# Kernel optimization log

Measured on AMD Instinct MI355X. Metric: run time of the kernel, lower is better.

The kernel has to match this reference:

```python
import jax, jax.numpy as jnp
import numpy as np
jax.config.update("jax_enable_x64", True)

T, C, F = 2048, 2048, 8192
f32 = jnp.float32
f64 = jnp.float64


def setup_inputs() -> dict:
    key = jax.random.key(0)
    ks = jax.random.split(key, 20)
    s = 0.02
    return {
        "x": jax.random.normal(ks[0], (T, C), f32),
        "att_shift": jnp.zeros((C,), f32),
        "wkv_state": jnp.zeros((2, C), f32),
        "ffn_shift": jnp.zeros((C,), f32),
        "ln1_w": jnp.ones((C,), f32),
        "ln1_b": jnp.zeros((C,), f32),
        "ln2_w": jnp.ones((C,), f32),
        "ln2_b": jnp.zeros((C,), f32),
        "time_mix_k": jax.random.uniform(ks[1], (C,), f32),
        "time_mix_v": jax.random.uniform(ks[2], (C,), f32),
        "time_mix_r": jax.random.uniform(ks[3], (C,), f32),
        "time_decay": jax.random.normal(ks[4], (C,), f32) * 0.5,
        "time_first": jax.random.normal(ks[5], (C,), f32) * 0.5,
        "att_key": jax.random.normal(ks[6], (C, C), f32) * s,
        "att_value": jax.random.normal(ks[7], (C, C), f32) * s,
        "att_receptance": jax.random.normal(ks[8], (C, C), f32) * s,
        "att_output": jax.random.normal(ks[9], (C, C), f32) * s,
        "ffn_time_mix_k": jax.random.uniform(ks[10], (C,), f32),
        "ffn_time_mix_r": jax.random.uniform(ks[11], (C,), f32),
        "ffn_key": jax.random.normal(ks[12], (F, C), f32) * s,
        "ffn_value": jax.random.normal(ks[13], (C, F), f32) * s,
        "ffn_receptance": jax.random.normal(ks[14], (C, C), f32) * s,
    }


def _ln(x, w, b):
    m = x.mean(-1, keepdims=True)
    v = x.var(-1, keepdims=True)
    return (x - m) * jax.lax.rsqrt(v + 1e-5) * w + b


def _wkv(time_decay, time_first, k, v, wkv_state):
    # faithful to wkv_mop: double-precision math, float32 state round-trip per step
    u = time_first.astype(f64)
    w = -jnp.exp(time_decay.astype(f64))
    ew = jnp.exp(w)

    def step(carry, kv_t):
        a, b = carry  # float32 states [C]
        k_t, v_t = kv_t
        kd = k_t.astype(f64)
        vd = v_t.astype(f64)
        e = jnp.exp(u + w + kd)
        y = (a + e * vd) / (b + e)
        kk = jnp.exp(kd)
        a2 = ((a + kk * vd) * ew).astype(f32)
        b2 = ((b + kk) * ew).astype(f32)
        return (a2, b2), y.astype(f32)

    _, y = jax.lax.scan(step, (wkv_state[0], wkv_state[1]), (k, v))
    return y  # [T, C]


def reference(x, att_shift, wkv_state, ffn_shift, ln1_w, ln1_b, ln2_w, ln2_b,
              time_mix_k, time_mix_v, time_mix_r, time_decay, time_first,
              att_key, att_value, att_receptance, att_output,
              ffn_time_mix_k, ffn_time_mix_r, ffn_key, ffn_value, ffn_receptance):
    # --- TimeMix (att) on rx = ln1(x); shiftamount=2 -> prev token of rx ---
    rx = _ln(x, ln1_w, ln1_b)                         # [T, C]
    xx = jnp.concatenate([att_shift[None, :], rx[:-1]], axis=0)
    xk = rx * time_mix_k + xx * (1.0 - time_mix_k)
    xv = rx * time_mix_v + xx * (1.0 - time_mix_v)
    xr = rx * time_mix_r + xx * (1.0 - time_mix_r)
    k = xk @ att_key.T                                # [T, C]
    v = xv @ att_value.T
    sr = jax.nn.sigmoid(xr @ att_receptance.T)
    y = _wkv(time_decay, time_first, k, v, wkv_state)
    x = x + (sr * y) @ att_output.T
    # --- ChannelMix (ffn) on fx = ln2(x); shift = prev token of fx ---
    fx = _ln(x, ln2_w, ln2_b)
    fxx = jnp.concatenate([ffn_shift[None, :], fx[:-1]], axis=0)
    fk = fx * ffn_time_mix_k + fxx * (1.0 - ffn_time_mix_k)
    fr = fx * ffn_time_mix_r + fxx * (1.0 - ffn_time_mix_r)
    kf = jnp.square(jax.nn.relu(fk @ ffn_key.T))      # [T, F]
    kv = kf @ ffn_value.T                             # [T, C]
    out = x + jax.nn.sigmoid(fr @ ffn_receptance.T) * kv
    return out
```

## Files before the change

kernel.cpp:

```cpp
#include <hip/hip_runtime.h>
#include <hip/hip_bf16.h>

typedef unsigned short u16;
typedef short bf16x8 __attribute__((ext_vector_type(8)));
typedef float f32x4 __attribute__((ext_vector_type(4)));

#define T_DIM 2048
#define C_DIM 2048
#define F_DIM 8192
#define WKV_L 32
#define WKV_P (T_DIM / WKV_L)

__device__ __forceinline__ u16 f2bf(float f) {
    unsigned int u = __float_as_uint(f);
    u += 0x7fff + ((u >> 16) & 1);
    return (u16)(u >> 16);
}

__device__ __forceinline__ void async16(const void* g, void* l) {
    __builtin_amdgcn_global_load_lds(
        (__attribute__((address_space(1))) const unsigned int*)g,
        (__attribute__((address_space(3))) unsigned int*)l, 16, 0, 0);
}

__global__ __launch_bounds__(256) void ln_mix3(
        const float* __restrict__ x, const float* __restrict__ sh,
        const float* __restrict__ w, const float* __restrict__ b,
        const float* __restrict__ mk, const float* __restrict__ mv,
        const float* __restrict__ mr,
        u16* __restrict__ xk, u16* __restrict__ xv, u16* __restrict__ xr) {
    __shared__ float red[16];
    const int t = blockIdx.x, tid = threadIdx.x;
    const float4* cr = (const float4*)(x + (size_t)t * C_DIM);
    float4 c0 = cr[tid * 2], c1 = cr[tid * 2 + 1];
    float s = c0.x + c0.y + c0.z + c0.w + c1.x + c1.y + c1.z + c1.w;
    float q = c0.x * c0.x + c0.y * c0.y + c0.z * c0.z + c0.w * c0.w
            + c1.x * c1.x + c1.y * c1.y + c1.z * c1.z + c1.w * c1.w;
    float4 p0, p1;
    float sp = 0.f, qp = 0.f;
    if (t > 0) {
        const float4* pr = (const float4*)(x + (size_t)(t - 1) * C_DIM);
        p0 = pr[tid * 2]; p1 = pr[tid * 2 + 1];
        sp = p0.x + p0.y + p0.z + p0.w + p1.x + p1.y + p1.z + p1.w;
        qp = p0.x * p0.x + p0.y * p0.y + p0.z * p0.z + p0.w * p0.w
           + p1.x * p1.x + p1.y * p1.y + p1.z * p1.z + p1.w * p1.w;
    } else {
        const float4* pr = (const float4*)sh;
        p0 = pr[tid * 2]; p1 = pr[tid * 2 + 1];
    }
    #pragma unroll
    for (int off = 32; off > 0; off >>= 1) {
        s += __shfl_down(s, off);   q += __shfl_down(q, off);
        sp += __shfl_down(sp, off); qp += __shfl_down(qp, off);
    }
    const int lane = tid & 63, wv = tid >> 6;
    if (lane == 0) { red[wv] = s; red[4 + wv] = q; red[8 + wv] = sp; red[12 + wv] = qp; }
    __syncthreads();
    if (tid == 0) {
        red[0] += red[1] + red[2] + red[3];
        red[4] += red[5] + red[6] + red[7];
        red[8] += red[9] + red[10] + red[11];
        red[12] += red[13] + red[14] + red[15];
    }
    __syncthreads();
    const float mc = red[0] * (1.f / C_DIM);
    const float ic = rsqrtf(red[4] * (1.f / C_DIM) - mc * mc + 1e-5f);
    const float mp = red[8] * (1.f / C_DIM);
    const float ip = rsqrtf(red[12] * (1.f / C_DIM) - mp * mp + 1e-5f);
    const float4* w4 = (const float4*)w;
    const float4* b4 = (const float4*)b;
    #pragma unroll
    for (int j = 0; j < 2; ++j) {
        const int i4 = tid * 2 + j;
        float4 cv = j ? c1 : c0, pv = j ? p1 : p0;
        float4 wv4 = w4[i4], bv = b4[i4];
        float4 cl, pl;
        cl.x = (cv.x - mc) * ic * wv4.x + bv.x;
        cl.y = (cv.y - mc) * ic * wv4.y + bv.y;
        cl.z = (cv.z - mc) * ic * wv4.z + bv.z;
        cl.w = (cv.w - mc) * ic * wv4.w + bv.w;
        if (t > 0) {
            pl.x = (pv.x - mp) * ip * wv4.x + bv.x;
            pl.y = (pv.y - mp) * ip * wv4.y + bv.y;
            pl.z = (pv.z - mp) * ip * wv4.z + bv.z;
            pl.w = (pv.w - mp) * ip * wv4.w + bv.w;
        } else pl = pv;
        const size_t o = (size_t)t * (C_DIM / 4) + i4;
        float4 m;
        ushort4 r;
        m = ((const float4*)mk)[i4];
        r.x = f2bf(cl.x * m.x + pl.x * (1.f - m.x));
        r.y = f2bf(cl.y * m.y + pl.y * (1.f - m.y));
        r.z = f2bf(cl.z * m.z + pl.z * (1.f - m.z));
        r.w = f2bf(cl.w * m.w + pl.w * (1.f - m.w));
        ((ushort4*)xk)[o] = r;
        m = ((const float4*)mv)[i4];
        r.x = f2bf(cl.x * m.x + pl.x * (1.f - m.x));
        r.y = f2bf(cl.y * m.y + pl.y * (1.f - m.y));
        r.z = f2bf(cl.z * m.z + pl.z * (1.f - m.z));
        r.w = f2bf(cl.w * m.w + pl.w * (1.f - m.w));
        ((ushort4*)xv)[o] = r;
        m = ((const float4*)mr)[i4];
        r.x = f2bf(cl.x * m.x + pl.x * (1.f - m.x));
        r.y = f2bf(cl.y * m.y + pl.y * (1.f - m.y));
        r.z = f2bf(cl.z * m.z + pl.z * (1.f - m.z));
        r.w = f2bf(cl.w * m.w + pl.w * (1.f - m.w));
        ((ushort4*)xr)[o] = r;
    }
}

__global__ __launch_bounds__(256) void ln_mix2(
        const float* __restrict__ x, const float* __restrict__ sh,
        const float* __restrict__ w, const float* __restrict__ b,
        const float* __restrict__ mk, const float* __restrict__ mr,
        u16* __restrict__ fk, u16* __restrict__ fr) {
    __shared__ float red[16];
    const int t = blockIdx.x, tid = threadIdx.x;
    const float4* cr = (const float4*)(x + (size_t)t * C_DIM);
    float4 c0 = cr[tid * 2], c1 = cr[tid * 2 + 1];
    float s = c0.x + c0.y + c0.z + c0.w + c1.x + c1.y + c1.z + c1.w;
    float q = c0.x * c0.x + c0.y * c0.y + c0.z * c0.z + c0.w * c0.w
            + c1.x * c1.x + c1.y * c1.y + c1.z * c1.z + c1.w * c1.w;
    float4 p0, p1;
    float sp = 0.f, qp = 0.f;
    if (t > 0) {
        const float4* pr = (const float4*)(x + (size_t)(t - 1) * C_DIM);
        p0 = pr[tid * 2]; p1 = pr[tid * 2 + 1];
        sp = p0.x + p0.y + p0.z + p0.w + p1.x + p1.y + p1.z + p1.w;
        qp = p0.x * p0.x + p0.y * p0.y + p0.z * p0.z + p0.w * p0.w
           + p1.x * p1.x + p1.y * p1.y + p1.z * p1.z + p1.w * p1.w;
    } else {
        const float4* pr = (const float4*)sh;
        p0 = pr[tid * 2]; p1 = pr[tid * 2 + 1];
    }
    #pragma unroll
    for (int off = 32; off > 0; off >>= 1) {
        s += __shfl_down(s, off);   q += __shfl_down(q, off);
        sp += __shfl_down(sp, off); qp += __shfl_down(qp, off);
    }
    const int lane = tid & 63, wv = tid >> 6;
    if (lane == 0) { red[wv] = s; red[4 + wv] = q; red[8 + wv] = sp; red[12 + wv] = qp; }
    __syncthreads();
    if (tid == 0) {
        red[0] += red[1] + red[2] + red[3];
        red[4] += red[5] + red[6] + red[7];
        red[8] += red[9] + red[10] + red[11];
        red[12] += red[13] + red[14] + red[15];
    }
    __syncthreads();
    const float mc = red[0] * (1.f / C_DIM);
    const float ic = rsqrtf(red[4] * (1.f / C_DIM) - mc * mc + 1e-5f);
    const float mp = red[8] * (1.f / C_DIM);
    const float ip = rsqrtf(red[12] * (1.f / C_DIM) - mp * mp + 1e-5f);
    const float4* w4 = (const float4*)w;
    const float4* b4 = (const float4*)b;
    #pragma unroll
    for (int j = 0; j < 2; ++j) {
        const int i4 = tid * 2 + j;
        float4 cv = j ? c1 : c0, pv = j ? p1 : p0;
        float4 wv4 = w4[i4], bv = b4[i4];
        float4 cl, pl;
        cl.x = (cv.x - mc) * ic * wv4.x + bv.x;
        cl.y = (cv.y - mc) * ic * wv4.y + bv.y;
        cl.z = (cv.z - mc) * ic * wv4.z + bv.z;
        cl.w = (cv.w - mc) * ic * wv4.w + bv.w;
        if (t > 0) {
            pl.x = (pv.x - mp) * ip * wv4.x + bv.x;
            pl.y = (pv.y - mp) * ip * wv4.y + bv.y;
            pl.z = (pv.z - mp) * ip * wv4.z + bv.z;
            pl.w = (pv.w - mp) * ip * wv4.w + bv.w;
        } else pl = pv;
        const size_t o = (size_t)t * (C_DIM / 4) + i4;
        float4 m;
        ushort4 r;
        m = ((const float4*)mk)[i4];
        r.x = f2bf(cl.x * m.x + pl.x * (1.f - m.x));
        r.y = f2bf(cl.y * m.y + pl.y * (1.f - m.y));
        r.z = f2bf(cl.z * m.z + pl.z * (1.f - m.z));
        r.w = f2bf(cl.w * m.w + pl.w * (1.f - m.w));
        ((ushort4*)fk)[o] = r;
        m = ((const float4*)mr)[i4];
        r.x = f2bf(cl.x * m.x + pl.x * (1.f - m.x));
        r.y = f2bf(cl.y * m.y + pl.y * (1.f - m.y));
        r.z = f2bf(cl.z * m.z + pl.z * (1.f - m.z));
        r.w = f2bf(cl.w * m.w + pl.w * (1.f - m.w));
        ((ushort4*)fr)[o] = r;
    }
}

__global__ __launch_bounds__(256) void cvt_bf16(const float* __restrict__ in,
                                                u16* __restrict__ out, int n8) {
    int i = blockIdx.x * 256 + threadIdx.x;
    const int stride = gridDim.x * 256;
    for (; i < n8; i += stride) {
        const float4* p = (const float4*)(in + (size_t)i * 8);
        float4 a = p[0], b = p[1];
        ushort4 lo, hi;
        lo.x = f2bf(a.x); lo.y = f2bf(a.y); lo.z = f2bf(a.z); lo.w = f2bf(a.w);
        hi.x = f2bf(b.x); hi.y = f2bf(b.y); hi.z = f2bf(b.z); hi.w = f2bf(b.w);
        ((ushort4*)out)[i * 2] = lo;
        ((ushort4*)out)[i * 2 + 1] = hi;
    }
}

__global__ __launch_bounds__(256) void cvt4_bf16(const float* __restrict__ i0,
                                                 const float* __restrict__ i1,
                                                 const float* __restrict__ i2,
                                                 const float* __restrict__ i3,
                                                 u16* __restrict__ out, int n8) {
    const int sel = blockIdx.y;
    const float* in = sel == 0 ? i0 : (sel == 1 ? i1 : (sel == 2 ? i2 : i3));
    u16* o = out + (size_t)sel * n8 * 8;
    int i = blockIdx.x * 256 + threadIdx.x;
    const int stride = gridDim.x * 256;
    for (; i < n8; i += stride) {
        const float4* p = (const float4*)(in + (size_t)i * 8);
        float4 a = p[0], b = p[1];
        ushort4 lo, hi;
        lo.x = f2bf(a.x); lo.y = f2bf(a.y); lo.z = f2bf(a.z); lo.w = f2bf(a.w);
        hi.x = f2bf(b.x); hi.y = f2bf(b.y); hi.z = f2bf(b.z); hi.w = f2bf(b.w);
        ((ushort4*)o)[i * 2] = lo;
        ((ushort4*)o)[i * 2 + 1] = hi;
    }
}

__global__ __launch_bounds__(256) void reduce2(const float* __restrict__ p0,
                                               const float* __restrict__ p1,
                                               float* __restrict__ o, int n4) {
    int i = blockIdx.x * 256 + threadIdx.x;
    const int stride = gridDim.x * 256;
    for (; i < n4; i += stride) {
        float4 a = ((const float4*)p0)[i], b = ((const float4*)p1)[i];
        float4 r;
        r.x = a.x + b.x;
        r.y = a.y + b.y;
        r.z = a.z + b.z;
        r.w = a.w + b.w;
        ((float4*)o)[i] = r;
    }
}

__global__ __launch_bounds__(256) void wkv_part(const float* __restrict__ td,
                                                const float* __restrict__ k,
                                                const float* __restrict__ v,
                                                float* __restrict__ Ab,
                                                float* __restrict__ Bb) {
    const int idx = blockIdx.x * 256 + threadIdx.x;
    const int c = idx & (C_DIM - 1);
    const int p = idx >> 11;
    const float ew = expf(-expf(td[c]));
    float A = 0.f, B = 0.f;
    size_t o = (size_t)(p * WKV_L) * C_DIM + c;
    #pragma unroll 4
    for (int i = 0; i < WKV_L; ++i, o += C_DIM) {
        const float kk = expf(k[o]);
        A = (A + kk * v[o]) * ew;
        B = (B + kk) * ew;
    }
    Ab[p * C_DIM + c] = A;
    Bb[p * C_DIM + c] = B;
}

__global__ __launch_bounds__(256) void wkv_comb(const float* __restrict__ td,
                                                const float* __restrict__ st,
                                                const float* __restrict__ Ab,
                                                const float* __restrict__ Bb,
                                                float* __restrict__ Sa,
                                                float* __restrict__ Sb) {
    const int c = blockIdx.x * 256 + threadIdx.x;
    const float w = -expf(td[c]);
    const float dL = expf(w * (float)WKV_L);
    float a = st[c];
    float b = st[C_DIM + c];
    #pragma unroll 4
    for (int p = 0; p < WKV_P; ++p) {
        Sa[p * C_DIM + c] = a;
        Sb[p * C_DIM + c] = b;
        a = dL * a + Ab[p * C_DIM + c];
        b = dL * b + Bb[p * C_DIM + c];
    }
}

__global__ __launch_bounds__(256) void wkv_emit(const float* __restrict__ td,
                                                const float* __restrict__ tf,
                                                const float* __restrict__ k,
                                                const float* __restrict__ v,
                                                const float* __restrict__ r,
                                                const float* __restrict__ Sa,
                                                const float* __restrict__ Sb,
                                                u16* __restrict__ pout) {
    const int idx = blockIdx.x * 256 + threadIdx.x;
    const int c = idx & (C_DIM - 1);
    const int p = idx >> 11;
    const float u = tf[c];
    const float w = -expf(td[c]);
    const float ew = expf(w);
    float a = Sa[p * C_DIM + c];
    float b = Sb[p * C_DIM + c];
    size_t o = (size_t)(p * WKV_L) * C_DIM + c;
    #pragma unroll 2
    for (int i = 0; i < WKV_L; ++i, o += C_DIM) {
        const float kt = k[o], vt = v[o], rt = r[o];
        const float e = expf(u + w + kt);
        const float y = (a + e * vt) / (b + e);
        const float kk = expf(kt);
        a = (a + kk * vt) * ew;
        b = (b + kk) * ew;
        const float sr = 1.f / (1.f + expf(-rt));
        pout[o] = f2bf(sr * y);
    }
}

enum { EPI_F32 = 0, EPI_ADDX = 1, EPI_RELU2 = 2, EPI_SIGMULADD = 3 };

template <int EPI>
__global__ __launch_bounds__(256, 3) void gemm_bt(
        const u16* __restrict__ A, int lda, long a_zs,
        const u16* __restrict__ B, int ldb, long b_zs,
        long koff, int Kloop,
        void* __restrict__ outp, int ldo, long o_zs,
        const float* __restrict__ aux1, const float* __restrict__ aux2) {
    __shared__ u16 lds[3 * 8192];
    const int tid = threadIdx.x;
    const int l = tid & 63, w = tid >> 6;
    const int wr2 = w >> 1, wc2 = w & 1;

    const int gx = gridDim.x, gy = gridDim.y;
    const int nxy = gx * gy;
    const int flat = (blockIdx.z * gy + blockIdx.y) * gx + blockIdx.x;
    const int cpx = (nxy * gridDim.z) >> 3;
    const int swz = (flat & 7) * cpx + (flat >> 3);
    const int z = swz / nxy;
    const int rem = swz - z * nxy;
    const int bm = rem % gy;
    const int bn = rem / gy;

    const u16* Ag = A + (size_t)z * a_zs + (size_t)z * koff + (size_t)bm * 128 * lda;
    const u16* Bg = B + (size_t)z * b_zs + (size_t)z * koff + (size_t)bn * 128 * ldb;

    long gA[2], gB[2];
    int dA[2], dB[2];
    #pragma unroll
    for (int j = 0; j < 2; ++j) {
        const int off = j * 4096 + w * 1024 + l * 16;
        const int row = off >> 6;
        const int cb = (off & 63) ^ (((off >> 9) & 1) << 5);
        gA[j] = (long)row * lda + (cb >> 1);
        gB[j] = (long)row * ldb + (cb >> 1);
        dA[j] = j * 2048 + w * 512;
        dB[j] = 4096 + j * 2048 + w * 512;
    }

    int offA[4], offB[4];
    #pragma unroll
    for (int m = 0; m < 4; ++m) {
        const int lin = (wr2 * 64 + m * 16 + (l & 15)) * 64 + ((l >> 4) << 4);
        offA[m] = (lin ^ (((lin >> 9) & 1) << 5)) >> 1;
    }
    #pragma unroll
    for (int n = 0; n < 4; ++n) {
        const int lin = (wc2 * 64 + n * 16 + (l & 15)) * 64 + ((l >> 4) << 4);
        offB[n] = 4096 + ((lin ^ (((lin >> 9) & 1) << 5)) >> 1);
    }

    const f32x4 fz = {0.f, 0.f, 0.f, 0.f};
    f32x4 acc[4][4];
    #pragma unroll
    for (int m = 0; m < 4; ++m)
        #pragma unroll
        for (int n = 0; n < 4; ++n) acc[m][n] = fz;

    const int NT = Kloop >> 5;

    auto stage = [&](int kt, int sp) {
        const long ko = (long)kt << 5;
        const int sb = sp * 8192;
        async16(Ag + gA[0] + ko, &lds[sb + dA[0]]);
        async16(Ag + gA[1] + ko, &lds[sb + dA[1]]);
        async16(Bg + gB[0] + ko, &lds[sb + dB[0]]);
        async16(Bg + gB[1] + ko, &lds[sb + dB[1]]);
    };

    stage(0, 0);
    stage(1, 1);

    int sr = 0;
    for (int t = 0; t < NT; ++t) {
        asm volatile("s_waitcnt vmcnt(4)" ::: "memory");
        __builtin_amdgcn_s_barrier();
        __builtin_amdgcn_sched_barrier(0);
        {
            const int tp = (t + 2 < NT) ? t + 2 : NT - 1;
            const int sp = (sr == 0) ? 2 : sr - 1;
            stage(tp, sp);
        }
        const int sb = sr * 8192;
        bf16x8 af[4], bfv[4];
        #pragma unroll
        for (int m = 0; m < 4; ++m) af[m] = *(const bf16x8*)&lds[sb + offA[m]];
        #pragma unroll
        for (int n = 0; n < 4; ++n) bfv[n] = *(const bf16x8*)&lds[sb + offB[n]];
        __builtin_amdgcn_s_setprio(1);
        #pragma unroll
        for (int m = 0; m < 2; ++m)
            #pragma unroll
            for (int n = 0; n < 4; ++n)
                acc[m][n] = __builtin_amdgcn_mfma_f32_16x16x32_bf16(af[m], bfv[n], acc[m][n], 0, 0, 0);
        __builtin_amdgcn_s_setprio(0);
        __builtin_amdgcn_s_setprio(1);
        #pragma unroll
        for (int m = 2; m < 4; ++m)
            #pragma unroll
            for (int n = 0; n < 4; ++n)
                acc[m][n] = __builtin_amdgcn_mfma_f32_16x16x32_bf16(af[m], bfv[n], acc[m][n], 0, 0, 0);
        __builtin_amdgcn_s_setprio(0);
        sr = (sr == 2) ? 0 : sr + 1;
    }
    asm volatile("s_waitcnt vmcnt(0)" ::: "memory");

    const int r00 = bm * 128 + wr2 * 64 + ((l >> 4) << 2);
    const int c00 = bn * 128 + wc2 * 64 + (l & 15);
    #pragma unroll
    for (int m = 0; m < 4; ++m) {
        #pragma unroll
        for (int n = 0; n < 4; ++n) {
            #pragma unroll
            for (int j = 0; j < 4; ++j) {
                const int rr = r00 + m * 16 + j;
                const int cc = c00 + n * 16;
                const size_t o = (size_t)rr * ldo + cc;
                const float val = acc[m][n][j];
                if constexpr (EPI == EPI_F32) {
                    ((float*)outp)[(size_t)z * o_zs + o] = val;
                } else if constexpr (EPI == EPI_ADDX) {
                    ((float*)outp)[o] = aux1[o] + val;
                } else if constexpr (EPI == EPI_RELU2) {
                    const float tp2 = fmaxf(val, 0.f);
                    ((u16*)outp)[o] = f2bf(tp2 * tp2);
                } else {
                    const float sg = 1.f / (1.f + expf(-val));
                    ((float*)outp)[o] = aux1[o] + sg * aux2[o];
                }
            }
        }
    }
}

extern "C" void kernel_launch(void* const* d_in, const int* in_sizes, int n_in,
                              void* d_out, int out_size, void* d_ws, size_t ws_size,
                              hipStream_t stream) {
    const float* x         = (const float*)d_in[0];
    const float* att_shift = (const float*)d_in[1];
    const float* wkv_state = (const float*)d_in[2];
    const float* ffn_shift = (const float*)d_in[3];
    const float* ln1w = (const float*)d_in[4];
    const float* ln1b = (const float*)d_in[5];
    const float* ln2w = (const float*)d_in[6];
    const float* ln2b = (const float*)d_in[7];
    const float* tmk  = (const float*)d_in[8];
    const float* tmv  = (const float*)d_in[9];
    const float* tmr  = (const float*)d_in[10];
    const float* td   = (const float*)d_in[11];
    const float* tf   = (const float*)d_in[12];
    const float* Wk   = (const float*)d_in[13];
    const float* Wv   = (const float*)d_in[14];
    const float* Wr   = (const float*)d_in[15];
    const float* Wo   = (const float*)d_in[16];
    const float* ftmk = (const float*)d_in[17];
    const float* ftmr = (const float*)d_in[18];
    const float* Wfk  = (const float*)d_in[19];
    const float* Wfv  = (const float*)d_in[20];
    const float* Wfr  = (const float*)d_in[21];
    float* out = (float*)d_out;

    char* ws = (char*)d_ws;
    const size_t MB = 1ull << 20;
    float* rx0 = (float*)(ws + 0);
    u16*   xk  = (u16*)(ws + 16 * MB);
    u16*   xv  = (u16*)(ws + 24 * MB);
    u16*   xr  = (u16*)(ws + 32 * MB);
    float* kb  = (float*)(ws + 40 * MB);
    float* vb  = (float*)(ws + 56 * MB);
    float* rb  = (float*)(ws + 72 * MB);
    u16*   pb  = (u16*)(ws + 88 * MB);
    float* x1  = (float*)(ws + 96 * MB);
    u16*   kf  = (u16*)(ws + 112 * MB);
    u16*   Wb  = (u16*)(ws + 144 * MB);
    float* wAb = (float*)(ws + 112 * MB);
    float* wBb = (float*)(ws + 112 * MB + 512 * 1024);
    float* wSa = (float*)(ws + 113 * MB);
    float* wSb = (float*)(ws + 113 * MB + 512 * 1024);
    float* fvp = (float*)(ws + 32 * MB);

    const int T = T_DIM, C = C_DIM, F = F_DIM;
    const dim3 blk(256);

    ln_mix3<<<T, blk, 0, stream>>>(x, att_shift, ln1w, ln1b, tmk, tmv, tmr, xk, xv, xr);

    cvt4_bf16<<<dim3(1024, 4), blk, 0, stream>>>(Wk, Wv, Wr, Wo, Wb, C * C / 8);
    gemm_bt<EPI_F32><<<dim3(C / 128, T / 128, 3), blk, 0, stream>>>(
        xk, C, (long)T * C, Wb, C, (long)C * C, 0, C,
        kb, C, (long)T * C, nullptr, nullptr);

    wkv_part<<<(C * WKV_P) / 256, blk, 0, stream>>>(td, kb, vb, wAb, wBb);
    wkv_comb<<<C / 256, blk, 0, stream>>>(td, wkv_state, wAb, wBb, wSa, wSb);
    wkv_emit<<<(C * WKV_P) / 256, blk, 0, stream>>>(td, tf, kb, vb, rb, wSa, wSb, pb);

    gemm_bt<EPI_ADDX><<<dim3(C / 128, T / 128, 1), blk, 0, stream>>>(
        pb, C, 0, Wb + 3 * (size_t)C * C, C, 0, 0, C, x1, C, 0, x, nullptr);

    ln_mix2<<<T, blk, 0, stream>>>(x1, ffn_shift, ln2w, ln2b, ftmk, ftmr, xk, xv);

    cvt_bf16<<<2048, blk, 0, stream>>>(Wfk, Wb, F * C / 8);
    gemm_bt<EPI_RELU2><<<dim3(F / 128, T / 128, 1), blk, 0, stream>>>(
        xk, C, 0, Wb, C, 0, 0, C, kf, F, 0, nullptr, nullptr);

    cvt_bf16<<<2048, blk, 0, stream>>>(Wfv, Wb, C * F / 8);
    gemm_bt<EPI_F32><<<dim3(C / 128, T / 128, 2), blk, 0, stream>>>(
        kf, F, 0, Wb, F, 0, 4096, 4096, fvp, C, (long)T * C, nullptr, nullptr);
    reduce2<<<2048, blk, 0, stream>>>(fvp, fvp + (size_t)T * C, rx0, T * C / 4);

    cvt_bf16<<<2048, blk, 0, stream>>>(Wfr, Wb, C * C / 8);
    gemm_bt<EPI_SIGMULADD><<<dim3(C / 128, T / 128, 1), blk, 0, stream>>>(
        xv, C, 0, Wb, C, 0, 0, C, out, C, 0, x1, rx0);
}
```

Baseline: 412.3 us.

## Add 256x256 8-wave pipelined GEMM for FFN matmuls with 4-way split-K

Adds a new bf16 MFMA GEMM kernel for the two large FFN matmuls. It uses 256x256 output tiles, 512 threads and double-buffered LDS fed by async global-to-LDS loads. It interleaves LDS fragment reads, staging of the next K tile and MFMA quads under barriers and raised wave priority, and swizzles the block order across groups of 8. The ffn_value GEMM moves from 2-way to 4-way split-K to keep enough blocks with the larger tiles, and a reduce4 kernel sums the four partials. The cost is extra partial-buffer traffic, a larger workspace footprint and heavy register use from 32 accumulators per lane.

```diff
diff --git a/kernel.cpp b/kernel.cpp
--- a/kernel.cpp
+++ b/kernel.cpp
@@ -224,18 +224,21 @@
     }
 }
 
-__global__ __launch_bounds__(256) void reduce2(const float* __restrict__ p0,
+__global__ __launch_bounds__(256) void reduce4(const float* __restrict__ p0,
                                                const float* __restrict__ p1,
+                                               const float* __restrict__ p2,
+                                               const float* __restrict__ p3,
                                                float* __restrict__ o, int n4) {
     int i = blockIdx.x * 256 + threadIdx.x;
     const int stride = gridDim.x * 256;
     for (; i < n4; i += stride) {
         float4 a = ((const float4*)p0)[i], b = ((const float4*)p1)[i];
+        float4 c = ((const float4*)p2)[i], d = ((const float4*)p3)[i];
         float4 r;
-        r.x = a.x + b.x;
-        r.y = a.y + b.y;
-        r.z = a.z + b.z;
-        r.w = a.w + b.w;
+        r.x = a.x + b.x + c.x + d.x;
+        r.y = a.y + b.y + c.y + d.y;
+        r.z = a.z + b.z + c.z + d.z;
+        r.w = a.w + b.w + c.w + d.w;
         ((float4*)o)[i] = r;
     }
 }
@@ -446,6 +449,181 @@
     }
 }
 
+template <int EPI>
+__global__ __launch_bounds__(512, 2) void gemm8p(
+        const u16* __restrict__ A, int lda,
+        const u16* __restrict__ B, int ldb,
+        long koff, int Kloop,
+        void* __restrict__ outp, int ldo, long o_zs) {
+    __shared__ u16 lds[65536];
+    const int tid = threadIdx.x;
+    const int l = tid & 63, w = tid >> 6;
+    const int wm = w >> 2, wn = w & 3;
+
+    const int gx = gridDim.x, gy = gridDim.y;
+    const int nxy = gx * gy;
+    const int flat = (blockIdx.z * gy + blockIdx.y) * gx + blockIdx.x;
+    const int cpx = (nxy * gridDim.z) >> 3;
+    const int swz = (flat & 7) * cpx + (flat >> 3);
+    const int z = swz / nxy;
+    const int rem = swz - z * nxy;
+    const int bm = rem % gy;
+    const int bn = rem / gy;
+
+    const u16* Ag = A + (size_t)z * koff + (size_t)bm * 256 * lda;
+    const u16* Bg = B + (size_t)z * koff + (size_t)bn * 256 * ldb;
+
+    long srcA[4], srcB[4];
+    int dst[4];
+    #pragma unroll
+    for (int hj = 0; hj < 4; ++hj) {
+        const int off = (hj >> 1) * 16384 + (hj & 1) * 8192 + w * 1024 + l * 16;
+        const int e = off ^ (((off >> 9) & 1) << 5);
+        srcA[hj] = (long)(e >> 7) * lda + ((e & 127) >> 1);
+        srcB[hj] = (long)(e >> 7) * ldb + ((e & 127) >> 1);
+        dst[hj] = off >> 1;
+    }
+
+    int offA[2][4], offB0[4];
+    #pragma unroll
+    for (int mh = 0; mh < 2; ++mh)
+        #pragma unroll
+        for (int mi = 0; mi < 4; ++mi) {
+            const int row = wm * 128 + (mh * 4 + mi) * 16 + (l & 15);
+            const int lin = row * 128 + ((l >> 4) << 4);
+            offA[mh][mi] = (lin ^ (((lin >> 9) & 1) << 5)) >> 1;
+        }
+    #pragma unroll
+    for (int n = 0; n < 4; ++n) {
+        const int row = wn * 64 + n * 16 + (l & 15);
+        const int lin = row * 128 + ((l >> 4) << 4);
+        offB0[n] = 16384 + ((lin ^ (((lin >> 9) & 1) << 5)) >> 1);
+    }
+
+    const f32x4 fz = {0.f, 0.f, 0.f, 0.f};
+    f32x4 acc[8][4];
+    #pragma unroll
+    for (int m = 0; m < 8; ++m)
+        #pragma unroll
+        for (int n = 0; n < 4; ++n) acc[m][n] = fz;
+
+    const int NT = Kloop >> 6;
+    const int NP = NT >> 1;
+
+    auto stgA = [&](int kt, int buf, int h) {
+        const long ko = (long)kt << 6;
+        #pragma unroll
+        for (int j = 0; j < 2; ++j)
+            async16(Ag + srcA[h * 2 + j] + ko, &lds[buf * 32768 + dst[h * 2 + j]]);
+    };
+    auto stgB = [&](int kt, int buf, int h) {
+        const long ko = (long)kt << 6;
+        #pragma unroll
+        for (int j = 0; j < 2; ++j)
+            async16(Bg + srcB[h * 2 + j] + ko, &lds[buf * 32768 + 16384 + dst[h * 2 + j]]);
+    };
+
+#define PH_OPEN() __builtin_amdgcn_s_barrier(); \
+    asm volatile("s_waitcnt lgkmcnt(0)" ::: "memory"); \
+    __builtin_amdgcn_sched_barrier(0)
+#define QUAD(af, bf, MO) \
+    __builtin_amdgcn_s_setprio(1); \
+    _Pragma("unroll") \
+    for (int mi = 0; mi < 4; ++mi) \
+        _Pragma("unroll") \
+        for (int n = 0; n < 4; ++n) \
+            acc[MO + mi][n] = __builtin_amdgcn_mfma_f32_16x16x32_bf16((af)[mi], (bf)[n], acc[MO + mi][n], 0, 0, 0); \
+    __builtin_amdgcn_s_setprio(0)
+
+    stgA(0, 0, 0); stgA(0, 0, 1); stgB(0, 0, 0); stgB(0, 0, 1);
+    stgA(1, 1, 0);
+    asm volatile("s_waitcnt vmcnt(2)" ::: "memory");
+    __builtin_amdgcn_s_barrier();
+
+    for (int p = 0; p < NP; ++p) {
+        const int kt1 = 2 * p + 1;
+        const int kn0 = (2 * p + 2 < NT) ? 2 * p + 2 : NT - 1;
+        const int kn1 = (2 * p + 3 < NT) ? 2 * p + 3 : NT - 1;
+        bf16x8 a0[4], a1[4], a0k[4], a1k[4], bb[4];
+        #pragma unroll
+        for (int mi = 0; mi < 4; ++mi) a0[mi] = *(const bf16x8*)&lds[offA[0][mi]];
+        #pragma unroll
+        for (int n = 0; n < 4; ++n) bb[n] = *(const bf16x8*)&lds[offB0[n]];
+        stgA(kt1, 1, 1);
+        PH_OPEN(); QUAD(a0, bb, 0);
+        __builtin_amdgcn_s_barrier();
+        #pragma unroll
+        for (int mi = 0; mi < 4; ++mi) a1[mi] = *(const bf16x8*)&lds[offA[1][mi]];
+        #pragma unroll
+        for (int mi = 0; mi < 4; ++mi) a0k[mi] = *(const bf16x8*)&lds[offA[0][mi] + 32];
+        stgB(kt1, 1, 0);
+        PH_OPEN(); QUAD(a1, bb, 4);
+        __builtin_amdgcn_s_barrier();
+        #pragma unroll
+        for (int n = 0; n < 4; ++n) bb[n] = *(const bf16x8*)&lds[offB0[n] + 32];
+        #pragma unroll
+        for (int mi = 0; mi < 4; ++mi) a1k[mi] = *(const bf16x8*)&lds[offA[1][mi] + 32];
+        stgB(kt1, 1, 1);
+        PH_OPEN(); QUAD(a0k, bb, 0);
+        __builtin_amdgcn_s_barrier();
+        stgA(kn0, 0, 0);
+        PH_OPEN(); QUAD(a1k, bb, 4);
+        asm volatile("s_waitcnt vmcnt(2)" ::: "memory");
+        __builtin_amdgcn_s_barrier();
+        #pragma unroll
+        for (int mi = 0; mi < 4; ++mi) a0[mi] = *(const bf16x8*)&lds[32768 + offA[0][mi]];
+        #pragma unroll
+        for (int n = 0; n < 4; ++n) bb[n] = *(const bf16x8*)&lds[32768 + offB0[n]];
+        stgA(kn0, 0, 1);
+        PH_OPEN(); QUAD(a0, bb, 0);
+        __builtin_amdgcn_s_barrier();
+        #pragma unroll
+        for (int mi = 0; mi < 4; ++mi) a1[mi] = *(const bf16x8*)&lds[32768 + offA[1][mi]];
+        #pragma unroll
+        for (int mi = 0; mi < 4; ++mi) a0k[mi] = *(const bf16x8*)&lds[32768 + offA[0][mi] + 32];
+        stgB(kn0, 0, 0);
+        PH_OPEN(); QUAD(a1, bb, 4);
+        __builtin_amdgcn_s_barrier();
+        #pragma unroll
+        for (int n = 0; n < 4; ++n) bb[n] = *(const bf16x8*)&lds[32768 + offB0[n] + 32];
+        #pragma unroll
+        for (int mi = 0; mi < 4; ++mi) a1k[mi] = *(const bf16x8*)&lds[32768 + offA[1][mi] + 32];
+        stgB(kn0, 0, 1);
+        PH_OPEN(); QUAD(a0k, bb, 0);
+        __builtin_amdgcn_s_barrier();
+        stgA(kn1, 1, 0);
+        PH_OPEN(); QUAD(a1k, bb, 4);
+        asm volatile("s_waitcnt vmcnt(2)" ::: "memory");
+        __builtin_amdgcn_s_barrier();
+    }
+    asm volatile("s_waitcnt vmcnt(0)" ::: "memory");
+
+#undef PH_OPEN
+#undef QUAD
+
+    const int r00 = bm * 256 + wm * 128 + ((l >> 4) << 2);
+    const int c00 = bn * 256 + wn * 64 + (l & 15);
+    #pragma unroll
+    for (int m = 0; m < 8; ++m) {
+        #pragma unroll
+        for (int n = 0; n < 4; ++n) {
+            #pragma unroll
+            for (int j = 0; j < 4; ++j) {
+                const int rr = r00 + m * 16 + j;
+                const int cc = c00 + n * 16;
+                const size_t o = (size_t)rr * ldo + cc;
+                const float val = acc[m][n][j];
+                if constexpr (EPI == EPI_F32) {
+                    ((float*)outp)[(size_t)z * o_zs + o] = val;
+                } else {
+                    const float tp2 = fmaxf(val, 0.f);
+                    ((u16*)outp)[o] = f2bf(tp2 * tp2);
+                }
+            }
+        }
+    }
+}
+
 extern "C" void kernel_launch(void* const* d_in, const int* in_sizes, int n_in,
                               void* d_out, int out_size, void* d_ws, size_t ws_size,
                               hipStream_t stream) {
@@ -493,7 +671,7 @@
     float* fvp = (float*)(ws + 32 * MB);
 
     const int T = T_DIM, C = C_DIM, F = F_DIM;
-    const dim3 blk(256);
+    const dim3 blk(256), blk5(512);
 
     ln_mix3<<<T, blk, 0, stream>>>(x, att_shift, ln1w, ln1b, tmk, tmv, tmr, xk, xv, xr);
 
@@ -512,13 +690,14 @@
     ln_mix2<<<T, blk, 0, stream>>>(x1, ffn_shift, ln2w, ln2b, ftmk, ftmr, xk, xv);
 
     cvt_bf16<<<2048, blk, 0, stream>>>(Wfk, Wb, F * C / 8);
-    gemm_bt<EPI_RELU2><<<dim3(F / 128, T / 128, 1), blk, 0, stream>>>(
-        xk, C, 0, Wb, C, 0, 0, C, kf, F, 0, nullptr, nullptr);
+    gemm8p<EPI_RELU2><<<dim3(F / 256, T / 256, 1), blk5, 0, stream>>>(
+        xk, C, Wb, C, 0, C, kf, F, 0);
 
     cvt_bf16<<<2048, blk, 0, stream>>>(Wfv, Wb, C * F / 8);
-    gemm_bt<EPI_F32><<<dim3(C / 128, T / 128, 2), blk, 0, stream>>>(
-        kf, F, 0, Wb, F, 0, 4096, 4096, fvp, C, (long)T * C, nullptr, nullptr);
-    reduce2<<<2048, blk, 0, stream>>>(fvp, fvp + (size_t)T * C, rx0, T * C / 4);
+    gemm8p<EPI_F32><<<dim3(C / 256, T / 256, 4), blk5, 0, stream>>>(
+        kf, F, Wb, F, 2048, 2048, fvp, C, (long)T * C);
+    reduce4<<<2048, blk, 0, stream>>>(fvp, fvp + (size_t)T * C, fvp + 2 * (size_t)T * C,
+                                      fvp + 3 * (size_t)T * C, rx0, T * C / 4);
 
     cvt_bf16<<<2048, blk, 0, stream>>>(Wfr, Wb, C * C / 8);
     gemm_bt<EPI_SIGMULADD><<<dim3(C / 128, T / 128, 1), blk, 0, stream>>>(
```

Result: faster. 388.1 us (-5.9%).
